# Performance work log

Hardware: AMD Instinct MI355X
Metric: run time of the kernel (lower is better)

The kernel has to match this reference:

```python
import jax, jax.numpy as jnp
import numpy as np

B, S, DM, NH, DK, DFF = 4, 2048, 512, 8, 64, 2048
EPS = 1e-5


def setup_inputs() -> dict:
    key = jax.random.key(0)
    ks = jax.random.split(key, 16)
    sd = 1.0 / np.sqrt(DM)
    inp = {
        'x': jax.random.normal(ks[0], (B, S, DM), dtype=jnp.float32),
        'wq': jax.random.normal(ks[1], (DM, DM), dtype=jnp.float32) * sd,
        'bq': jnp.zeros((DM,), dtype=jnp.float32),
        'wk': jax.random.normal(ks[2], (DM, DM), dtype=jnp.float32) * sd,
        'bk': jnp.zeros((DM,), dtype=jnp.float32),
        'wv': jax.random.normal(ks[3], (DM, DM), dtype=jnp.float32) * sd,
        'bv': jnp.zeros((DM,), dtype=jnp.float32),
        'wo': jax.random.normal(ks[4], (DM, DM), dtype=jnp.float32) * sd,
        'bo': jnp.zeros((DM,), dtype=jnp.float32),
        'ln_g': jnp.ones((DM,), dtype=jnp.float32),
        'ln_b': jnp.zeros((DM,), dtype=jnp.float32),
        'w1': jax.random.normal(ks[5], (DFF, DM), dtype=jnp.float32) * sd,
        'b1': jnp.zeros((DFF,), dtype=jnp.float32),
        'w2': jax.random.normal(ks[6], (DM, DFF), dtype=jnp.float32) * (1.0 / np.sqrt(DFF)),
        'b2': jnp.zeros((DM,), dtype=jnp.float32),
    }
    return inp


def _layernorm(x, g, b):
    mu = jnp.mean(x, axis=-1, keepdims=True)
    var = jnp.mean(jnp.square(x - mu), axis=-1, keepdims=True)
    return (x - mu) * jax.lax.rsqrt(var + EPS) * g + b


def reference(x, wq, bq, wk, bk, wv, bv, wo, bo, ln_g, ln_b, w1, b1, w2, b2):
    # projections (torch Linear: y = x @ W.T + b)
    q = x @ wq.T + bq
    k = x @ wk.T + bk
    v = x @ wv.T + bv
    # chunk along feature dim into NH heads of size DK
    q = q.reshape(B, S, NH, DK)
    k = k.reshape(B, S, NH, DK)
    v = v.reshape(B, S, NH, DK)
    scores = jnp.einsum('bihd,bjhd->bhij', q, k) / np.sqrt(DK)  # [B,NH,S,S]
    probs = jax.nn.softmax(scores, axis=-1)
    o = jnp.einsum('bhij,bjhd->bihd', probs, v).reshape(B, S, DM)
    o = o @ wo.T + bo
    # residual + shared layernorm (dropout p=0 -> identity)
    h = _layernorm(o + x, ln_g, ln_b)
    ff = jax.nn.relu(h @ w1.T + b1) @ w2.T + b2
    return _layernorm(ff + h, ln_g, ln_b)
```

## Files before the change

kernel.cpp:

```cpp
#include <hip/hip_runtime.h>

typedef __attribute__((ext_vector_type(8))) short short8;
typedef __attribute__((ext_vector_type(8))) unsigned short ushort8;
typedef __attribute__((ext_vector_type(4))) unsigned short ushort4v;
typedef __attribute__((ext_vector_type(4))) float f32x4;
typedef __attribute__((ext_vector_type(16))) float f32x16;

#define DEV static __device__ __forceinline__

DEV unsigned short f2bf(float f) {
  unsigned u = __builtin_bit_cast(unsigned, f);
  u += 0x7fffu + ((u >> 16) & 1u);
  return (unsigned short)(u >> 16);
}

DEV float bf2f(unsigned short u) {
  return __builtin_bit_cast(float, (unsigned)u << 16);
}

DEV void gload_lds16(const void* g, void* l) {
  __builtin_amdgcn_global_load_lds((__attribute__((address_space(1))) void*)g,
                                   (__attribute__((address_space(3))) void*)l,
                                   16, 0, 0);
}

DEV unsigned cvtpk(float lo, float hi) {
  unsigned u;
  asm("v_cvt_pk_bf16_f32 %0, %1, %2" : "=v"(u) : "v"(lo), "v"(hi));
  return u;
}

DEV void pl32(unsigned& a, unsigned& b) {
  asm("v_permlane32_swap_b32 %0, %1" : "+v"(a), "+v"(b));
}

DEV short8 pack4(unsigned a, unsigned b, unsigned c, unsigned d) {
  int4 t = make_int4((int)a, (int)b, (int)c, (int)d);
  return __builtin_bit_cast(short8, t);
}

__global__ __launch_bounds__(256) void cvt_all_k(
    const float4* __restrict__ wq, const float4* __restrict__ wk,
    const float4* __restrict__ wv, const float4* __restrict__ wo,
    const float4* __restrict__ w1, const float4* __restrict__ w2,
    const float4* __restrict__ x, ushort4v* __restrict__ wqkv,
    ushort4v* __restrict__ wob, ushort4v* __restrict__ w1b,
    ushort4v* __restrict__ w2b, ushort4v* __restrict__ xb) {
  const int i = threadIdx.x;
  const int b = blockIdx.x;
  const float4* s;
  ushort4v* d;
  size_t u;
  if (b < 256)       { s = wq; d = wqkv;          u = (size_t)b * 256 + i; }
  else if (b < 512)  { s = wk; d = wqkv + 65536;  u = (size_t)(b - 256) * 256 + i; }
  else if (b < 768)  { s = wv; d = wqkv + 131072; u = (size_t)(b - 512) * 256 + i; }
  else if (b < 1024) { s = wo; d = wob;           u = (size_t)(b - 768) * 256 + i; }
  else if (b < 2048) { s = w1; d = w1b;           u = (size_t)(b - 1024) * 256 + i; }
  else if (b < 3072) { s = w2; d = w2b;           u = (size_t)(b - 2048) * 256 + i; }
  else               { s = x;  d = xb;            u = (size_t)(b - 3072) * 256 + i; }
  float4 v = s[u];
  ushort4v o = { f2bf(v.x), f2bf(v.y), f2bf(v.z), f2bf(v.w) };
  d[u] = o;
}

__global__ void pack_bias_k(const float* __restrict__ bq, const float* __restrict__ bk,
                            const float* __restrict__ bv, float* __restrict__ o) {
  int i = threadIdx.x;
  o[i] = bq[i];
  o[512 + i] = bk[i];
  o[1024 + i] = bv[i];
}

template <int EPI>
__global__ __launch_bounds__(256) void gemm_bt(
    const unsigned short* __restrict__ A, const unsigned short* __restrict__ Bw,
    const float* __restrict__ bias, int M, int N, int K,
    unsigned short* __restrict__ outb, float* __restrict__ outf,
    const unsigned short* __restrict__ residb) {
  __shared__ __align__(16) unsigned short As[128 * 64];
  __shared__ __align__(16) unsigned short Bs[128 * 64];
  const int tid = threadIdx.x;
  const int lane = tid & 63;
  const int wv = tid >> 6;
  const int wr = wv >> 1, wc = wv & 1;
  const int lrow = lane & 15, lgrp = lane >> 4;
  const int bm = blockIdx.x * 128;
  const int bn = blockIdx.y * 128;

  f32x4 acc[4][4];
#pragma unroll
  for (int m = 0; m < 4; m++)
#pragma unroll
    for (int n = 0; n < 4; n++) acc[m][n] = (f32x4){0.f, 0.f, 0.f, 0.f};

  for (int k0 = 0; k0 < K; k0 += 64) {
    __syncthreads();
#pragma unroll
    for (int i = 0; i < 4; i++) {
      const int sb = wv * 64 + i * 256;
      const int slot = sb + lane;
      const int row = slot >> 3;
      const int cc = (slot & 7) ^ (row & 7);
      gload_lds16(A + (size_t)(bm + row) * K + k0 + cc * 8, &As[sb * 8]);
      gload_lds16(Bw + (size_t)(bn + row) * K + k0 + cc * 8, &Bs[sb * 8]);
    }
    __syncthreads();

#pragma unroll
    for (int kk = 0; kk < 2; kk++) {
      short8 af[4], bfr[4];
#pragma unroll
      for (int m = 0; m < 4; m++) {
        const int row = wr * 64 + m * 16 + lrow;
        af[m] = *(const short8*)&As[row * 64 + (((lgrp + 4 * kk) ^ (row & 7)) * 8)];
      }
#pragma unroll
      for (int n = 0; n < 4; n++) {
        const int row = wc * 64 + n * 16 + lrow;
        bfr[n] = *(const short8*)&Bs[row * 64 + (((lgrp + 4 * kk) ^ (row & 7)) * 8)];
      }
#pragma unroll
      for (int m = 0; m < 4; m++)
#pragma unroll
        for (int n = 0; n < 4; n++)
          acc[m][n] = __builtin_amdgcn_mfma_f32_16x16x32_bf16(af[m], bfr[n], acc[m][n], 0, 0, 0);
    }
  }

  if constexpr (EPI == 0) {
    const int proj = bn >> 9;
    if (proj == 2) {
      __shared__ __align__(16) unsigned short VT[128 * 136];
#pragma unroll
      for (int n = 0; n < 4; n++) {
        const int cl = wc * 64 + n * 16 + lrow;
        const float bval = bias[bn + cl];
#pragma unroll
        for (int m = 0; m < 4; m++)
#pragma unroll
          for (int r = 0; r < 4; r++)
            VT[cl * 136 + wr * 64 + m * 16 + lgrp * 4 + r] = f2bf(acc[m][n][r] + bval);
      }
      __syncthreads();
      const int j = (bn - 1024) >> 7;
      const int b = bm >> 11;
      const int sbase = bm & 2047;
      unsigned short* vout = outb + (size_t)2 * 4194304;
#pragma unroll
      for (int q = 0; q < 8; q++) {
        const int chunk = q * 256 + tid;
        const int cl = chunk >> 4, s8 = chunk & 15;
        const int head = 2 * j + (cl >> 6), d = cl & 63;
        ushort8 val = *(const ushort8*)&VT[cl * 136 + s8 * 8];
        *(ushort8*)(vout + ((size_t)(b * 8 + head) * 64 + d) * 2048 + sbase + s8 * 8) = val;
      }
    } else {
      const float qs = (proj == 0) ? 0.18033688011f : 1.0f;
#pragma unroll
      for (int m = 0; m < 4; m++) {
#pragma unroll
        for (int n = 0; n < 4; n++) {
          const int gcol = bn + wc * 64 + n * 16 + lrow;
          const float bval = bias[gcol];
          const int feat = gcol & 511;
          const int head = feat >> 6, d = feat & 63;
#pragma unroll
          for (int r = 0; r < 4; r++) {
            const int grow = bm + wr * 64 + m * 16 + lgrp * 4 + r;
            const int b = grow >> 11, s = grow & 2047;
            const int bh = b * 8 + head;
            outb[(size_t)proj * 4194304 + ((size_t)bh * 2048 + s) * 64 + d] =
                f2bf((acc[m][n][r] + bval) * qs);
          }
        }
      }
    }
  } else {
#pragma unroll
    for (int m = 0; m < 4; m++) {
#pragma unroll
      for (int n = 0; n < 4; n++) {
        const int gcol = bn + wc * 64 + n * 16 + lrow;
        const float bval = bias[gcol];
#pragma unroll
        for (int r = 0; r < 4; r++) {
          const int grow = bm + wr * 64 + m * 16 + lgrp * 4 + r;
          float v = acc[m][n][r] + bval;
          const size_t o = (size_t)grow * N + gcol;
          if constexpr (EPI == 1) {
            outb[o] = f2bf(v + bf2f(residb[o]));
          } else if constexpr (EPI == 2) {
            outb[o] = f2bf(v > 0.f ? v : 0.f);
          } else {
            outf[o] = v + bf2f(residb[o]);
          }
        }
      }
    }
  }
}

template <int EPI>
__global__ __launch_bounds__(256) void gemm_n64(
    const unsigned short* __restrict__ A, const unsigned short* __restrict__ Bw,
    const float* __restrict__ bias, int M, int N, int K,
    unsigned short* __restrict__ outb, float* __restrict__ outf,
    const unsigned short* __restrict__ residb) {
  __shared__ __align__(16) unsigned short As[128 * 64];
  __shared__ __align__(16) unsigned short Bs[64 * 64];
  const int tid = threadIdx.x;
  const int lane = tid & 63;
  const int wv = tid >> 6;
  const int lrow = lane & 15, lgrp = lane >> 4;
  const int bm = blockIdx.x * 128;
  const int bn = blockIdx.y * 64;

  f32x4 acc[2][4];
#pragma unroll
  for (int m = 0; m < 2; m++)
#pragma unroll
    for (int n = 0; n < 4; n++) acc[m][n] = (f32x4){0.f, 0.f, 0.f, 0.f};

  for (int k0 = 0; k0 < K; k0 += 64) {
    __syncthreads();
#pragma unroll
    for (int i = 0; i < 4; i++) {
      const int sb = wv * 64 + i * 256;
      const int slot = sb + lane;
      const int row = slot >> 3;
      const int cc = (slot & 7) ^ (row & 7);
      gload_lds16(A + (size_t)(bm + row) * K + k0 + cc * 8, &As[sb * 8]);
    }
#pragma unroll
    for (int i = 0; i < 2; i++) {
      const int sb = wv * 64 + i * 256;
      const int slot = sb + lane;
      const int row = slot >> 3;
      const int cc = (slot & 7) ^ (row & 7);
      gload_lds16(Bw + (size_t)(bn + row) * K + k0 + cc * 8, &Bs[sb * 8]);
    }
    __syncthreads();

#pragma unroll
    for (int kk = 0; kk < 2; kk++) {
      short8 af[2], bfr[4];
#pragma unroll
      for (int m = 0; m < 2; m++) {
        const int row = wv * 32 + m * 16 + lrow;
        af[m] = *(const short8*)&As[row * 64 + (((lgrp + 4 * kk) ^ (row & 7)) * 8)];
      }
#pragma unroll
      for (int n = 0; n < 4; n++) {
        const int row = n * 16 + lrow;
        bfr[n] = *(const short8*)&Bs[row * 64 + (((lgrp + 4 * kk) ^ (row & 7)) * 8)];
      }
#pragma unroll
      for (int m = 0; m < 2; m++)
#pragma unroll
        for (int n = 0; n < 4; n++)
          acc[m][n] = __builtin_amdgcn_mfma_f32_16x16x32_bf16(af[m], bfr[n], acc[m][n], 0, 0, 0);
    }
  }

#pragma unroll
  for (int m = 0; m < 2; m++) {
#pragma unroll
    for (int n = 0; n < 4; n++) {
      const int gcol = bn + n * 16 + lrow;
      const float bval = bias[gcol];
#pragma unroll
      for (int r = 0; r < 4; r++) {
        const int grow = bm + wv * 32 + m * 16 + lgrp * 4 + r;
        float v = acc[m][n][r] + bval;
        const size_t o = (size_t)grow * N + gcol;
        if constexpr (EPI == 1) {
          outb[o] = f2bf(v + bf2f(residb[o]));
        } else {
          outf[o] = v + bf2f(residb[o]);
        }
      }
    }
  }
}

__global__ __launch_bounds__(256) void attn_k(
    const unsigned short* __restrict__ Qg, const unsigned short* __restrict__ Kg,
    const unsigned short* __restrict__ Vg, unsigned short* __restrict__ Og) {
  __shared__ __align__(16) unsigned short Kl[2][128 * 64];
  __shared__ __align__(16) unsigned short Vl[2][64 * 128];
  const int tid = threadIdx.x, lane = tid & 63, wq = tid >> 6;
  const int ql = lane & 31;
  const int hi = lane >> 5;
  const int bid = blockIdx.x;
  const int lin = (bid & 7) * 64 + (bid >> 3);
  const int bh = lin >> 4;
  const int q0 = (lin & 15) * 128;
  const int qw = q0 + wq * 32;
  const size_t hbase = (size_t)bh * (2048 * 64);

  int kR[4], kC[4], vR[4], vC[4];
#pragma unroll
  for (int i = 0; i < 4; i++) {
    const int slot = i * 256 + tid;
    kR[i] = slot >> 3;
    kC[i] = (slot & 7) ^ (kR[i] & 7);
    vR[i] = slot >> 4;
    vC[i] = (slot & 15) ^ (vR[i] & 15);
  }

  short8 qreg[4];
  {
    const unsigned short* qp = Qg + hbase + (size_t)(qw + ql) * 64 + hi * 8;
#pragma unroll
    for (int i = 0; i < 4; i++) qreg[i] = *(const short8*)(qp + 16 * i);
  }

  const unsigned one2 = 0x3F803F80u;
  const short8 ones = pack4(one2, one2, one2, one2);

  f32x16 oac0 = {0.f, 0.f, 0.f, 0.f, 0.f, 0.f, 0.f, 0.f,
                 0.f, 0.f, 0.f, 0.f, 0.f, 0.f, 0.f, 0.f};
  f32x16 oac1 = oac0;
  f32x16 lacc = oac0;

#pragma unroll
  for (int i = 0; i < 4; i++) {
    const int db = (i * 256 + wq * 64) * 8;
    gload_lds16(Kg + hbase + (size_t)kR[i] * 64 + kC[i] * 8, &Kl[0][db]);
    gload_lds16(Vg + hbase + (size_t)vR[i] * 2048 + vC[i] * 8, &Vl[0][db]);
  }
  __syncthreads();

  for (int it = 0; it < 16; ++it) {
    const int cur = it & 1;
    if (it < 15) {
      const int kt = (it + 1) * 128;
      const int nxt = cur ^ 1;
#pragma unroll
      for (int i = 0; i < 4; i++) {
        const int db = (i * 256 + wq * 64) * 8;
        gload_lds16(Kg + hbase + (size_t)(kt + kR[i]) * 64 + kC[i] * 8, &Kl[nxt][db]);
        gload_lds16(Vg + hbase + (size_t)vR[i] * 2048 + kt + vC[i] * 8, &Vl[nxt][db]);
      }
    }

#pragma unroll
    for (int hf = 0; hf < 2; hf++) {
      f32x16 sc0 = {0.f, 0.f, 0.f, 0.f, 0.f, 0.f, 0.f, 0.f,
                    0.f, 0.f, 0.f, 0.f, 0.f, 0.f, 0.f, 0.f};
      f32x16 sc1 = sc0;
      __builtin_amdgcn_s_setprio(1);
#pragma unroll
      for (int i = 0; i < 4; i++) {
        const int c8 = 2 * i + hi;
        const int r0 = hf * 64 + ql;
        const int r1 = hf * 64 + ql + 32;
        short8 ka = *(const short8*)&Kl[cur][(r0 * 8 + (c8 ^ (r0 & 7))) * 8];
        short8 kb = *(const short8*)&Kl[cur][(r1 * 8 + (c8 ^ (r1 & 7))) * 8];
        sc0 = __builtin_amdgcn_mfma_f32_32x32x16_bf16(ka, qreg[i], sc0, 0, 0, 0);
        sc1 = __builtin_amdgcn_mfma_f32_32x32x16_bf16(kb, qreg[i], sc1, 0, 0, 0);
      }
      __builtin_amdgcn_s_setprio(0);

      short8 pa[4];
#pragma unroll
      for (int t2 = 0; t2 < 2; t2++) {
        const f32x16& sc = t2 ? sc1 : sc0;
        float p[16];
#pragma unroll
        for (int r = 0; r < 16; r++) p[r] = __builtin_amdgcn_exp2f(sc[r]);
        unsigned w0a = cvtpk(p[0], p[1]),   w0b = cvtpk(p[2], p[3]);
        unsigned w1a = cvtpk(p[4], p[5]),   w1b = cvtpk(p[6], p[7]);
        unsigned w2a = cvtpk(p[8], p[9]),   w2b = cvtpk(p[10], p[11]);
        unsigned w3a = cvtpk(p[12], p[13]), w3b = cvtpk(p[14], p[15]);
        pl32(w0a, w1a);
        pl32(w0b, w1b);
        pa[2 * t2] = pack4(w0a, w0b, w1a, w1b);
        pl32(w2a, w3a);
        pl32(w2b, w3b);
        pa[2 * t2 + 1] = pack4(w2a, w2b, w3a, w3b);
      }

      __builtin_amdgcn_s_setprio(1);
#pragma unroll
      for (int ks = 0; ks < 4; ks++) {
        const int c8 = hf * 8 + 2 * ks + hi;
        const int r0 = ql;
        const int r1 = ql + 32;
        short8 vb0 = *(const short8*)&Vl[cur][(r0 * 16 + (c8 ^ (r0 & 15))) * 8];
        short8 vb1 = *(const short8*)&Vl[cur][(r1 * 16 + (c8 ^ (r1 & 15))) * 8];
        oac0 = __builtin_amdgcn_mfma_f32_32x32x16_bf16(pa[ks], vb0, oac0, 0, 0, 0);
        oac1 = __builtin_amdgcn_mfma_f32_32x32x16_bf16(pa[ks], vb1, oac1, 0, 0, 0);
        lacc = __builtin_amdgcn_mfma_f32_32x32x16_bf16(pa[ks], ones, lacc, 0, 0, 0);
      }
      __builtin_amdgcn_s_setprio(0);
    }

    __syncthreads();
  }

  const int b = bh >> 3, h = bh & 7;
#pragma unroll
  for (int r = 0; r < 16; r++) {
    const int qrow = (r & 3) + 8 * (r >> 2) + 4 * hi;
    const float invr = 1.0f / lacc[r];
    const size_t base = ((size_t)(b * 2048 + qw + qrow)) * 512 + h * 64 + ql;
    Og[base] = f2bf(oac0[r] * invr);
    Og[base + 32] = f2bf(oac1[r] * invr);
  }
}

__global__ __launch_bounds__(64) void ln_bf_k(const unsigned short* __restrict__ in,
                                              const float* __restrict__ g,
                                              const float* __restrict__ bb,
                                              unsigned short* __restrict__ out) {
  const int row = blockIdx.x, lane = threadIdx.x;
  ushort8 v = *(const ushort8*)(in + (size_t)row * 512 + lane * 8);
  float f[8];
#pragma unroll
  for (int j = 0; j < 8; j++) f[j] = bf2f(v[j]);
  float s = 0.f;
#pragma unroll
  for (int j = 0; j < 8; j++) s += f[j];
#pragma unroll
  for (int off = 32; off >= 1; off >>= 1) s += __shfl_xor(s, off);
  const float mu = s * (1.f / 512.f);
  float q = 0.f;
#pragma unroll
  for (int j = 0; j < 8; j++) { const float d = f[j] - mu; q += d * d; }
#pragma unroll
  for (int off = 32; off >= 1; off >>= 1) q += __shfl_xor(q, off);
  const float rstd = rsqrtf(q * (1.f / 512.f) + 1e-5f);
  const float4* gp = (const float4*)g;
  const float4* bp = (const float4*)bb;
  float4 g0 = gp[lane * 2], g1 = gp[lane * 2 + 1];
  float4 c0 = bp[lane * 2], c1 = bp[lane * 2 + 1];
  const float gg[8] = {g0.x, g0.y, g0.z, g0.w, g1.x, g1.y, g1.z, g1.w};
  const float cc[8] = {c0.x, c0.y, c0.z, c0.w, c1.x, c1.y, c1.z, c1.w};
  ushort8 ov;
#pragma unroll
  for (int j = 0; j < 8; j++) ov[j] = f2bf((f[j] - mu) * rstd * gg[j] + cc[j]);
  *(ushort8*)(out + (size_t)row * 512 + lane * 8) = ov;
}

__global__ __launch_bounds__(64) void ln_bf2f_k(const unsigned short* __restrict__ in,
                                                const float* __restrict__ g,
                                                const float* __restrict__ bb,
                                                float* __restrict__ outf) {
  const int row = blockIdx.x, lane = threadIdx.x;
  ushort8 v = *(const ushort8*)(in + (size_t)row * 512 + lane * 8);
  float f[8];
#pragma unroll
  for (int j = 0; j < 8; j++) f[j] = bf2f(v[j]);
  float s = 0.f;
#pragma unroll
  for (int j = 0; j < 8; j++) s += f[j];
#pragma unroll
  for (int off = 32; off >= 1; off >>= 1) s += __shfl_xor(s, off);
  const float mu = s * (1.f / 512.f);
  float q = 0.f;
#pragma unroll
  for (int j = 0; j < 8; j++) { const float d = f[j] - mu; q += d * d; }
#pragma unroll
  for (int off = 32; off >= 1; off >>= 1) q += __shfl_xor(q, off);
  const float rstd = rsqrtf(q * (1.f / 512.f) + 1e-5f);
  const float4* gp = (const float4*)g;
  const float4* bp = (const float4*)bb;
  float4 g0 = gp[lane * 2], g1 = gp[lane * 2 + 1];
  float4 c0 = bp[lane * 2], c1 = bp[lane * 2 + 1];
  const float gg[8] = {g0.x, g0.y, g0.z, g0.w, g1.x, g1.y, g1.z, g1.w};
  const float cc[8] = {c0.x, c0.y, c0.z, c0.w, c1.x, c1.y, c1.z, c1.w};
  float4 o0, o1;
  float* o0p = &o0.x;
  float* o1p = &o1.x;
#pragma unroll
  for (int j = 0; j < 4; j++) o0p[j] = (f[j] - mu) * rstd * gg[j] + cc[j];
#pragma unroll
  for (int j = 0; j < 4; j++) o1p[j] = (f[j + 4] - mu) * rstd * gg[j + 4] + cc[j + 4];
  float4* of = (float4*)(outf + (size_t)row * 512 + lane * 8);
  of[0] = o0;
  of[1] = o1;
}

extern "C" void kernel_launch(void* const* d_in, const int* in_sizes, int n_in,
                              void* d_out, int out_size, void* d_ws, size_t ws_size,
                              hipStream_t stream) {
  const float* x = (const float*)d_in[0];
  const float* wq = (const float*)d_in[1];
  const float* bq = (const float*)d_in[2];
  const float* wk = (const float*)d_in[3];
  const float* bk = (const float*)d_in[4];
  const float* wv = (const float*)d_in[5];
  const float* bv = (const float*)d_in[6];
  const float* wo = (const float*)d_in[7];
  const float* bo = (const float*)d_in[8];
  const float* ln_g = (const float*)d_in[9];
  const float* ln_b = (const float*)d_in[10];
  const float* w1 = (const float*)d_in[11];
  const float* b1 = (const float*)d_in[12];
  const float* w2 = (const float*)d_in[13];
  const float* b2 = (const float*)d_in[14];

  unsigned short* ws_u = (unsigned short*)d_ws;
  unsigned short* wqkv = ws_u;
  unsigned short* wob = wqkv + 786432;
  unsigned short* w1b = wob + 262144;
  unsigned short* w2b = w1b + 1048576;
  unsigned short* xb = w2b + 1048576;
  unsigned short* qb = xb + 4194304;
  unsigned short* kb = qb + 4194304;
  unsigned short* vtb = kb + 4194304;
  unsigned short* ob = vtb + 4194304;
  unsigned short* s1b = ob + 4194304;
  unsigned short* hb = s1b + 4194304;
  unsigned short* f1b = qb;
  float* bqkv = (float*)(hb + 4194304);

  cvt_all_k<<<7168, 256, 0, stream>>>(
      (const float4*)wq, (const float4*)wk, (const float4*)wv, (const float4*)wo,
      (const float4*)w1, (const float4*)w2, (const float4*)x,
      (ushort4v*)wqkv, (ushort4v*)wob, (ushort4v*)w1b, (ushort4v*)w2b,
      (ushort4v*)xb);
  pack_bias_k<<<1, 512, 0, stream>>>(bq, bk, bv, bqkv);

  gemm_bt<0><<<dim3(64, 12), 256, 0, stream>>>(xb, wqkv, bqkv, 8192, 1536, 512,
                                               qb, nullptr, nullptr);
  attn_k<<<512, 256, 0, stream>>>(qb, kb, vtb, ob);
  gemm_n64<1><<<dim3(64, 8), 256, 0, stream>>>(ob, wob, bo, 8192, 512, 512,
                                               s1b, nullptr, xb);
  ln_bf_k<<<8192, 64, 0, stream>>>(s1b, ln_g, ln_b, hb);
  gemm_bt<2><<<dim3(64, 16), 256, 0, stream>>>(hb, w1b, b1, 8192, 2048, 512,
                                               f1b, nullptr, nullptr);
  gemm_n64<1><<<dim3(64, 8), 256, 0, stream>>>(f1b, w2b, b2, 8192, 512, 2048,
                                               s1b, nullptr, hb);
  ln_bf2f_k<<<8192, 64, 0, stream>>>(s1b, ln_g, ln_b, (float*)d_out);
}
```

Measured before the change: 165.3 us.

## Restructure attention inner loop into full-tile QK and dual PV accumulators; fuse bias pack

The attention kernel now computes all four 32-row QK^T score tiles for the 128-key block at once instead of two halves. It then runs the PV MFMAs with two independent accumulator sets that are summed at the end, so back-to-back MFMAs do not depend on each other. It also sets launch_bounds(256,2) to target two blocks per CU. Separately, the bias-packing kernel is folded into the conversion kernel as an extra block, which removes one launch. The change adds register pressure (four score tiles plus six accumulators) while asking for higher occupancy, which risks spills.

```diff
diff --git a/kernel.cpp b/kernel.cpp
--- a/kernel.cpp
+++ b/kernel.cpp
@@ -45,9 +45,21 @@
     const float4* __restrict__ w1, const float4* __restrict__ w2,
     const float4* __restrict__ x, ushort4v* __restrict__ wqkv,
     ushort4v* __restrict__ wob, ushort4v* __restrict__ w1b,
-    ushort4v* __restrict__ w2b, ushort4v* __restrict__ xb) {
+    ushort4v* __restrict__ w2b, ushort4v* __restrict__ xb,
+    const float* __restrict__ bq, const float* __restrict__ bk,
+    const float* __restrict__ bv, float* __restrict__ bo) {
   const int i = threadIdx.x;
   const int b = blockIdx.x;
+  if (b >= 7168) {
+#pragma unroll
+    for (int j = 0; j < 2; j++) {
+      const int idx = j * 256 + i;
+      bo[idx] = bq[idx];
+      bo[512 + idx] = bk[idx];
+      bo[1024 + idx] = bv[idx];
+    }
+    return;
+  }
   const float4* s;
   ushort4v* d;
   size_t u;
@@ -61,14 +73,6 @@
   float4 v = s[u];
   ushort4v o = { f2bf(v.x), f2bf(v.y), f2bf(v.z), f2bf(v.w) };
   d[u] = o;
-}
-
-__global__ void pack_bias_k(const float* __restrict__ bq, const float* __restrict__ bk,
-                            const float* __restrict__ bv, float* __restrict__ o) {
-  int i = threadIdx.x;
-  o[i] = bq[i];
-  o[512 + i] = bk[i];
-  o[1024 + i] = bv[i];
 }
 
 template <int EPI>
@@ -283,7 +287,7 @@
   }
 }
 
-__global__ __launch_bounds__(256) void attn_k(
+__global__ __launch_bounds__(256, 2) void attn_k(
     const unsigned short* __restrict__ Qg, const unsigned short* __restrict__ Kg,
     const unsigned short* __restrict__ Vg, unsigned short* __restrict__ Og) {
   __shared__ __align__(16) unsigned short Kl[2][128 * 64];
@@ -318,10 +322,10 @@
   const unsigned one2 = 0x3F803F80u;
   const short8 ones = pack4(one2, one2, one2, one2);
 
-  f32x16 oac0 = {0.f, 0.f, 0.f, 0.f, 0.f, 0.f, 0.f, 0.f,
-                 0.f, 0.f, 0.f, 0.f, 0.f, 0.f, 0.f, 0.f};
-  f32x16 oac1 = oac0;
-  f32x16 lacc = oac0;
+  const f32x16 zz = {0.f, 0.f, 0.f, 0.f, 0.f, 0.f, 0.f, 0.f,
+                     0.f, 0.f, 0.f, 0.f, 0.f, 0.f, 0.f, 0.f};
+  f32x16 oA0 = zz, oA1 = zz, lA = zz;
+  f32x16 oB0 = zz, oB1 = zz, lB = zz;
 
 #pragma unroll
   for (int i = 0; i < 4; i++) {
@@ -344,57 +348,56 @@
       }
     }
 
-#pragma unroll
-    for (int hf = 0; hf < 2; hf++) {
-      f32x16 sc0 = {0.f, 0.f, 0.f, 0.f, 0.f, 0.f, 0.f, 0.f,
-                    0.f, 0.f, 0.f, 0.f, 0.f, 0.f, 0.f, 0.f};
-      f32x16 sc1 = sc0;
-      __builtin_amdgcn_s_setprio(1);
-#pragma unroll
-      for (int i = 0; i < 4; i++) {
-        const int c8 = 2 * i + hi;
-        const int r0 = hf * 64 + ql;
-        const int r1 = hf * 64 + ql + 32;
-        short8 ka = *(const short8*)&Kl[cur][(r0 * 8 + (c8 ^ (r0 & 7))) * 8];
-        short8 kb = *(const short8*)&Kl[cur][(r1 * 8 + (c8 ^ (r1 & 7))) * 8];
-        sc0 = __builtin_amdgcn_mfma_f32_32x32x16_bf16(ka, qreg[i], sc0, 0, 0, 0);
-        sc1 = __builtin_amdgcn_mfma_f32_32x32x16_bf16(kb, qreg[i], sc1, 0, 0, 0);
-      }
-      __builtin_amdgcn_s_setprio(0);
-
-      short8 pa[4];
-#pragma unroll
-      for (int t2 = 0; t2 < 2; t2++) {
-        const f32x16& sc = t2 ? sc1 : sc0;
-        float p[16];
-#pragma unroll
-        for (int r = 0; r < 16; r++) p[r] = __builtin_amdgcn_exp2f(sc[r]);
-        unsigned w0a = cvtpk(p[0], p[1]),   w0b = cvtpk(p[2], p[3]);
-        unsigned w1a = cvtpk(p[4], p[5]),   w1b = cvtpk(p[6], p[7]);
-        unsigned w2a = cvtpk(p[8], p[9]),   w2b = cvtpk(p[10], p[11]);
-        unsigned w3a = cvtpk(p[12], p[13]), w3b = cvtpk(p[14], p[15]);
-        pl32(w0a, w1a);
-        pl32(w0b, w1b);
-        pa[2 * t2] = pack4(w0a, w0b, w1a, w1b);
-        pl32(w2a, w3a);
-        pl32(w2b, w3b);
-        pa[2 * t2 + 1] = pack4(w2a, w2b, w3a, w3b);
-      }
-
-      __builtin_amdgcn_s_setprio(1);
-#pragma unroll
-      for (int ks = 0; ks < 4; ks++) {
-        const int c8 = hf * 8 + 2 * ks + hi;
-        const int r0 = ql;
-        const int r1 = ql + 32;
-        short8 vb0 = *(const short8*)&Vl[cur][(r0 * 16 + (c8 ^ (r0 & 15))) * 8];
-        short8 vb1 = *(const short8*)&Vl[cur][(r1 * 16 + (c8 ^ (r1 & 15))) * 8];
-        oac0 = __builtin_amdgcn_mfma_f32_32x32x16_bf16(pa[ks], vb0, oac0, 0, 0, 0);
-        oac1 = __builtin_amdgcn_mfma_f32_32x32x16_bf16(pa[ks], vb1, oac1, 0, 0, 0);
-        lacc = __builtin_amdgcn_mfma_f32_32x32x16_bf16(pa[ks], ones, lacc, 0, 0, 0);
-      }
-      __builtin_amdgcn_s_setprio(0);
-    }
+    f32x16 sc[4] = {zz, zz, zz, zz};
+    __builtin_amdgcn_s_setprio(1);
+#pragma unroll
+    for (int i = 0; i < 4; i++) {
+      const int c8 = 2 * i + hi;
+#pragma unroll
+      for (int t = 0; t < 4; t++) {
+        const int r = 32 * t + ql;
+        short8 ka = *(const short8*)&Kl[cur][(r * 8 + (c8 ^ (r & 7))) * 8];
+        sc[t] = __builtin_amdgcn_mfma_f32_32x32x16_bf16(ka, qreg[i], sc[t], 0, 0, 0);
+      }
+    }
+    __builtin_amdgcn_s_setprio(0);
+
+    short8 pa[8];
+#pragma unroll
+    for (int t = 0; t < 4; t++) {
+      float p[16];
+#pragma unroll
+      for (int r = 0; r < 16; r++) p[r] = __builtin_amdgcn_exp2f(sc[t][r]);
+      unsigned w0a = cvtpk(p[0], p[1]),   w0b = cvtpk(p[2], p[3]);
+      unsigned w1a = cvtpk(p[4], p[5]),   w1b = cvtpk(p[6], p[7]);
+      unsigned w2a = cvtpk(p[8], p[9]),   w2b = cvtpk(p[10], p[11]);
+      unsigned w3a = cvtpk(p[12], p[13]), w3b = cvtpk(p[14], p[15]);
+      pl32(w0a, w1a);
+      pl32(w0b, w1b);
+      pa[2 * t] = pack4(w0a, w0b, w1a, w1b);
+      pl32(w2a, w3a);
+      pl32(w2b, w3b);
+      pa[2 * t + 1] = pack4(w2a, w2b, w3a, w3b);
+    }
+
+    __builtin_amdgcn_s_setprio(1);
+#pragma unroll
+    for (int ks = 0; ks < 8; ks += 2) {
+      const int c8e = 2 * ks + hi;
+      const int c8o = 2 * (ks + 1) + hi;
+      const int r0 = ql, r1 = ql + 32;
+      short8 ve0 = *(const short8*)&Vl[cur][(r0 * 16 + (c8e ^ (r0 & 15))) * 8];
+      short8 ve1 = *(const short8*)&Vl[cur][(r1 * 16 + (c8e ^ (r1 & 15))) * 8];
+      short8 vo0 = *(const short8*)&Vl[cur][(r0 * 16 + (c8o ^ (r0 & 15))) * 8];
+      short8 vo1 = *(const short8*)&Vl[cur][(r1 * 16 + (c8o ^ (r1 & 15))) * 8];
+      oA0 = __builtin_amdgcn_mfma_f32_32x32x16_bf16(pa[ks], ve0, oA0, 0, 0, 0);
+      oA1 = __builtin_amdgcn_mfma_f32_32x32x16_bf16(pa[ks], ve1, oA1, 0, 0, 0);
+      lA = __builtin_amdgcn_mfma_f32_32x32x16_bf16(pa[ks], ones, lA, 0, 0, 0);
+      oB0 = __builtin_amdgcn_mfma_f32_32x32x16_bf16(pa[ks + 1], vo0, oB0, 0, 0, 0);
+      oB1 = __builtin_amdgcn_mfma_f32_32x32x16_bf16(pa[ks + 1], vo1, oB1, 0, 0, 0);
+      lB = __builtin_amdgcn_mfma_f32_32x32x16_bf16(pa[ks + 1], ones, lB, 0, 0, 0);
+    }
+    __builtin_amdgcn_s_setprio(0);
 
     __syncthreads();
   }
@@ -403,10 +406,10 @@
 #pragma unroll
   for (int r = 0; r < 16; r++) {
     const int qrow = (r & 3) + 8 * (r >> 2) + 4 * hi;
-    const float invr = 1.0f / lacc[r];
+    const float invr = 1.0f / (lA[r] + lB[r]);
     const size_t base = ((size_t)(b * 2048 + qw + qrow)) * 512 + h * 64 + ql;
-    Og[base] = f2bf(oac0[r] * invr);
-    Og[base + 32] = f2bf(oac1[r] * invr);
+    Og[base] = f2bf((oA0[r] + oB0[r]) * invr);
+    Og[base + 32] = f2bf((oA1[r] + oB1[r]) * invr);
   }
 }
 
@@ -516,12 +519,11 @@
   unsigned short* f1b = qb;
   float* bqkv = (float*)(hb + 4194304);
 
-  cvt_all_k<<<7168, 256, 0, stream>>>(
+  cvt_all_k<<<7169, 256, 0, stream>>>(
       (const float4*)wq, (const float4*)wk, (const float4*)wv, (const float4*)wo,
       (const float4*)w1, (const float4*)w2, (const float4*)x,
       (ushort4v*)wqkv, (ushort4v*)wob, (ushort4v*)w1b, (ushort4v*)w2b,
-      (ushort4v*)xb);
-  pack_bias_k<<<1, 512, 0, stream>>>(bq, bk, bv, bqkv);
+      (ushort4v*)xb, bq, bk, bv, bqkv);
 
   gemm_bt<0><<<dim3(64, 12), 256, 0, stream>>>(xb, wqkv, bqkv, 8192, 1536, 512,
                                                qb, nullptr, nullptr);
```

Measured after the change: 160.7 us. -2.8%, faster.
